# Optimization experiments

Measured on AMD Instinct MI355X. Metric: run time of the kernel, lower is better.

## Reference

```python
import jax, jax.numpy as jnp
import numpy as np

IO_EMB = 128; IO_HID = 512; ENC_HID = 1024
B = 256; N_IO = 4; L = 64; T = 32; NPROD = 64; VOCAB = 128


def setup_inputs() -> dict:
    key = jax.random.key(0)
    ks = jax.random.split(key, 16)
    s = 0.02
    return {
        'exs_toks': jax.random.randint(ks[0], (L, B * N_IO), 0, VOCAB),
        'cls_toks': jax.random.randint(ks[1], (L, B * N_IO), 0, VOCAB),
        'E_io': jax.random.normal(ks[2], (VOCAB, IO_EMB)) * s,
        'Wi_f': jax.random.normal(ks[3], (2 * IO_EMB, 4 * IO_HID)) * s,
        'Wh_f': jax.random.normal(ks[4], (IO_HID, 4 * IO_HID)) * s,
        'b_f': jnp.zeros((4 * IO_HID,)),
        'Wi_b': jax.random.normal(ks[5], (2 * IO_EMB, 4 * IO_HID)) * s,
        'Wh_b': jax.random.normal(ks[6], (IO_HID, 4 * IO_HID)) * s,
        'b_b': jnp.zeros((4 * IO_HID,)),
        'W_attn': jax.random.normal(ks[7], (ENC_HID, 2 * IO_HID)) * s,
        'W_comp': jax.random.normal(ks[8], (ENC_HID + 2 * IO_HID, NPROD)) * s,
        'b_comp': jnp.zeros((NPROD,)),
        'v_Wi': jax.random.normal(ks[9], (ENC_HID, 4 * ENC_HID)) * s,
        'v_Wh': jax.random.normal(ks[10], (ENC_HID, 4 * ENC_HID)) * s,
        'v_b': jnp.zeros((4 * ENC_HID,)),
        'field_emb': jax.random.normal(ks[11], (T, ENC_HID)) * s,
        'actions': jax.random.randint(ks[12], (B, T), 0, NPROD),
    }


def _lstm(x, Wi, Wh, b, reverse=False):
    # x: [L, N, D] -> hs [L, N, H], final (h, c)
    H = Wh.shape[0]
    N = x.shape[1]
    def step(carry, xt):
        h, c = carry
        g = xt @ Wi + h @ Wh + b
        i, f, gg, o = jnp.split(g, 4, axis=-1)
        c = jax.nn.sigmoid(f) * c + jax.nn.sigmoid(i) * jnp.tanh(gg)
        h = jax.nn.sigmoid(o) * jnp.tanh(c)
        return (h, c), h
    init = (jnp.zeros((N, H), x.dtype), jnp.zeros((N, H), x.dtype))
    (hT, cT), hs = jax.lax.scan(step, init, x, reverse=reverse)
    return hs, hT, cT


def reference(exs_toks, cls_toks, E_io, Wi_f, Wh_f, b_f, Wi_b, Wh_b, b_b,
              W_attn, W_comp, b_comp, v_Wi, v_Wh, v_b, field_emb, actions):
    # --- encode_io: concat exs/cls embeddings, run biLSTM ---
    x = jnp.concatenate([E_io[exs_toks], E_io[cls_toks]], axis=-1)  # [L, B*N_IO, 2*IO_EMB]
    hs_f, hTf, cTf = _lstm(x, Wi_f, Wh_f, b_f)
    hs_b, hTb, cTb = _lstm(x, Wi_b, Wh_b, b_b, reverse=True)
    ctx_vecs = jnp.concatenate([hs_f, hs_b], -1).reshape(L, B, N_IO, 2 * IO_HID)
    # init decoder state: max over io examples of final biLSTM state
    h0 = jnp.concatenate([hTf, hTb], -1).reshape(B, N_IO, ENC_HID).max(axis=1)
    c0 = jnp.concatenate([cTf, cTb], -1).reshape(B, N_IO, ENC_HID).max(axis=1)

    def dec_step(carry, xs):
        h, c, acc = carry
        x_t, a_t = xs  # field embedding [ENC_HID], action ids [B]
        # Luong attention over io context vecs, per io example, then max-pool
        q = h @ W_attn                               # [B, 2*IO_HID]
        scores = jnp.einsum('lbne,be->lbn', ctx_vecs, q)
        attn = jax.nn.softmax(scores, axis=0)
        ctx = jnp.einsum('lbn,lbne->bne', attn, ctx_vecs).max(axis=1)  # [B, 2*IO_HID]
        # per-node classifier (composite type module): negative log-prob of chosen prod
        logits = jnp.concatenate([h, ctx], -1) @ W_comp + b_comp
        logp = jax.nn.log_softmax(logits, axis=-1)
        acc = acc - logp[jnp.arange(B), a_t]
        # constructor update via v_lstm cell
        g = x_t @ v_Wi + h @ v_Wh + v_b
        i, f, gg, o = jnp.split(g, 4, axis=-1)
        c = jax.nn.sigmoid(f) * c + jax.nn.sigmoid(i) * jnp.tanh(gg)
        h = jax.nn.sigmoid(o) * jnp.tanh(c)
        return (h, c, acc), None

    init = (h0, c0, jnp.zeros((B,), h0.dtype))
    (_, _, total), _ = jax.lax.scan(dec_step, init, (field_emb, actions.T))
    return total  # [B] per-program negative log-likelihood
```

## Files before the change

### kernel.cpp

```cpp
#include <hip/hip_runtime.h>
#include <hip/hip_bf16.h>

typedef __bf16 bf16x8 __attribute__((ext_vector_type(8)));
typedef float  f32x4  __attribute__((ext_vector_type(4)));
typedef float  f32x2  __attribute__((ext_vector_type(2)));
typedef unsigned int u32x4 __attribute__((ext_vector_type(4)));
typedef unsigned short ushort_t;
static_assert(sizeof(bf16x8) == 16, "bf16x8 must be 16B");

#define DEV __device__ __forceinline__

DEV f32x4 mfma16(bf16x8 a, bf16x8 b, f32x4 c) {
    return __builtin_amdgcn_mfma_f32_16x16x32_bf16(a, b, c, 0, 0, 0);
}
DEV f32x4 mfma8(long a, long b, f32x4 c) {
    return __builtin_amdgcn_mfma_f32_16x16x32_fp8_fp8(a, b, c, 0, 0, 0);
}
DEV float sigm(float x)   { return 1.0f / (1.0f + __expf(-x)); }
DEV float tanh_f(float x) { return 2.0f / (1.0f + __expf(-2.0f * x)) - 1.0f; }

DEV void glds16(const __hip_bfloat16* g, __hip_bfloat16* l) {
    __builtin_amdgcn_global_load_lds(
        (const __attribute__((address_space(1))) unsigned int*)g,
        (__attribute__((address_space(3))) unsigned int*)l, 16, 0, 0);
}

DEV unsigned char f32_to_fp8(float v) {
    int p = __builtin_amdgcn_cvt_pk_fp8_f32(v, v, 0, false);
    return (unsigned char)(p & 0xFF);
}

__global__ __launch_bounds__(128) void kdetect(const unsigned int* __restrict__ raw,
                                               int* __restrict__ mode) {
    __shared__ int cnt;
    if (threadIdx.x == 0) cnt = 0;
    __syncthreads();
    unsigned int w = raw[threadIdx.x];
    unsigned short lo = (unsigned short)(w & 0xFFFFu);
    unsigned int f32bits = ((unsigned int)lo) << 16;
    float v;
    __builtin_memcpy(&v, &f32bits, 4);
    float a = fabsf(v);
    if (a >= 1e-4f && a <= 1.0f) atomicAdd(&cnt, 1);
    __syncthreads();
    if (threadIdx.x == 0) *mode = (cnt >= 64) ? 1 : 0;
}

__global__ __launch_bounds__(256) void kcvt_bf16(const void* __restrict__ src,
                                                 __hip_bfloat16* __restrict__ dst,
                                                 int n, const int* __restrict__ mode) {
    int i = blockIdx.x * 256 + threadIdx.x;
    if (i >= n) return;
    if (*mode) dst[i] = ((const __hip_bfloat16*)src)[i];
    else       dst[i] = __float2bfloat16(((const float*)src)[i]);
}

__global__ __launch_bounds__(256) void kcvt_f32(const void* __restrict__ src,
                                                float* __restrict__ dst,
                                                int n, const int* __restrict__ mode) {
    int i = blockIdx.x * 256 + threadIdx.x;
    if (i >= n) return;
    if (*mode) dst[i] = __bfloat162float(((const __hip_bfloat16*)src)[i]);
    else       dst[i] = ((const float*)src)[i];
}

__global__ __launch_bounds__(256) void ktranspose_cvt(const void* __restrict__ src,
                                                      __hip_bfloat16* __restrict__ out,
                                                      int R, int C,
                                                      const int* __restrict__ mode) {
    __shared__ float tile[64][65];
    int c0 = blockIdx.x * 64, r0 = blockIdx.y * 64;
    int tx = threadIdx.x & 63, ty = threadIdx.x >> 6;
    int m = *mode;
#pragma unroll
    for (int i = ty; i < 64; i += 4) {
        size_t ix = (size_t)(r0 + i) * C + (c0 + tx);
        tile[i][tx] = m ? __bfloat162float(((const __hip_bfloat16*)src)[ix])
                        : ((const float*)src)[ix];
    }
    __syncthreads();
#pragma unroll
    for (int i = ty; i < 64; i += 4)
        out[(size_t)(c0 + i) * R + (r0 + tx)] = __float2bfloat16(tile[tx][i]);
}

__global__ __launch_bounds__(256) void kprep_gtab(
    const __hip_bfloat16* __restrict__ E,
    const __hip_bfloat16* __restrict__ WiT,
    const float* __restrict__ bF,
    const float* __restrict__ bB,
    float* __restrict__ G)
{
    int dh = blockIdx.x >> 6;
    int dir = dh >> 1, half = dh & 1;
    int m0 = ((blockIdx.x >> 5) & 1) * 64;
    int n0 = (blockIdx.x & 31) * 64;
    int lane = threadIdx.x & 63, wid = threadIdx.x >> 6;
    int wrow = wid >> 1, wcol = wid & 1;
    int r16 = lane & 15, quad = lane >> 4;

    f32x4 acc[2][2] = {};
    const __hip_bfloat16* Ap = E + (size_t)(m0 + wrow * 32 + r16) * 128 + quad * 8;
    const __hip_bfloat16* Bp = WiT + (size_t)dir * 2048 * 256
                             + (size_t)(n0 + wcol * 32 + r16) * 256 + half * 128 + quad * 8;
#pragma unroll
    for (int kb = 0; kb < 128; kb += 32) {
        bf16x8 a0 = *(const bf16x8*)(Ap + kb);
        bf16x8 a1 = *(const bf16x8*)(Ap + 16 * 128 + kb);
        bf16x8 b0 = *(const bf16x8*)(Bp + kb);
        bf16x8 b1 = *(const bf16x8*)(Bp + 16 * 256 + kb);
        acc[0][0] = mfma16(a0, b0, acc[0][0]);
        acc[0][1] = mfma16(a0, b1, acc[0][1]);
        acc[1][0] = mfma16(a1, b0, acc[1][0]);
        acc[1][1] = mfma16(a1, b1, acc[1][1]);
    }
    const float* bias = dir ? bB : bF;
    float* Gt = G + (size_t)dh * 128 * 2048;
#pragma unroll
    for (int rt = 0; rt < 2; rt++)
#pragma unroll
        for (int ct = 0; ct < 2; ct++)
#pragma unroll
            for (int r = 0; r < 4; r++) {
                int mm = m0 + wrow * 32 + rt * 16 + quad * 4 + r;
                int j = n0 + wcol * 32 + ct * 16 + r16;
                float v = acc[rt][ct][r];
                if (half == 0) v += bias[j];
                int g = j >> 9, u = j & 511;
                Gt[((size_t)mm * 512 + u) * 4 + g] = v;
            }
}

__global__ __launch_bounds__(256) void kprep_vx(
    const __hip_bfloat16* __restrict__ fe,
    const __hip_bfloat16* __restrict__ vWiT,
    const float* __restrict__ vb,
    float* __restrict__ VX)
{
    int n0 = blockIdx.x * 128;
    int lane = threadIdx.x & 63, wid = threadIdx.x >> 6;
    int r16 = lane & 15, quad = lane >> 4;
    f32x4 acc[2][2] = {};
    const __hip_bfloat16* Ap = fe + (size_t)r16 * 1024 + quad * 8;
    const __hip_bfloat16* Bp = vWiT + (size_t)(n0 + wid * 32 + r16) * 1024 + quad * 8;
    for (int kb = 0; kb < 1024; kb += 32) {
        bf16x8 a0 = *(const bf16x8*)(Ap + kb);
        bf16x8 a1 = *(const bf16x8*)(Ap + 16 * 1024 + kb);
        bf16x8 b0 = *(const bf16x8*)(Bp + kb);
        bf16x8 b1 = *(const bf16x8*)(Bp + 16 * 1024 + kb);
        acc[0][0] = mfma16(a0, b0, acc[0][0]);
        acc[0][1] = mfma16(a0, b1, acc[0][1]);
        acc[1][0] = mfma16(a1, b0, acc[1][0]);
        acc[1][1] = mfma16(a1, b1, acc[1][1]);
    }
#pragma unroll
    for (int rt = 0; rt < 2; rt++)
#pragma unroll
        for (int ct = 0; ct < 2; ct++)
#pragma unroll
            for (int r = 0; r < 4; r++) {
                int m = rt * 16 + quad * 4 + r;
                int j = n0 + wid * 32 + ct * 16 + r16;
                VX[(size_t)m * 4096 + j] = acc[rt][ct][r] + vb[j];
            }
}

__global__ __launch_bounds__(256, 2) void kenc_step(
    int t,
    const __hip_bfloat16* __restrict__ WhT,
    const float* __restrict__ Gtab,
    const int* __restrict__ exs,
    const int* __restrict__ cls,
    const __hip_bfloat16* __restrict__ h_in,
    __hip_bfloat16* __restrict__ h_out,
    float* __restrict__ c_st,
    unsigned char* __restrict__ ctx8)
{
    __shared__ __align__(16) __hip_bfloat16 sA[3][64 * 64];
    __shared__ __align__(16) __hip_bfloat16 sB[3][128 * 64];

    int bid = blockIdx.x;
    int dir = bid >> 8;
    int mt  = (bid >> 4) & 15;
    int us  = bid & 15;
    int l = dir ? (63 - t) : t;
    int m0 = mt * 64, u0 = us * 32;

    int lane = threadIdx.x & 63, w = threadIdx.x >> 6;
    int wm = w >> 1, wu = w & 1;
    int r16 = lane & 15, quad = lane >> 4;
    int srow = lane >> 3;
    int scol = ((lane & 7) ^ srow) * 8;

    const __hip_bfloat16* Ab = h_in + (size_t)dir * 1024 * 512;
    const __hip_bfloat16* Bb = WhT + (size_t)dir * 2048 * 512;

    f32x4 acc[4][2] = {};

    auto stage = [&](int buf, int it) {
        int kb = it * 64;
#pragma unroll
        for (int c = 0; c < 2; c++) {
            int r8 = (w * 2 + c) * 8;
            glds16(Ab + (size_t)(m0 + r8 + srow) * 512 + kb + scol,
                   &sA[buf][r8 * 64]);
        }
#pragma unroll
        for (int c = 0; c < 4; c++) {
            int rl = (w * 4 + c) * 8;
            int rr = rl + srow;
            int g = rr >> 5, j = rr & 31;
            glds16(Bb + (size_t)(g * 512 + u0 + j) * 512 + kb + scol,
                   &sB[buf][rl * 64]);
        }
    };

    stage(0, 0);
    stage(1, 1);

    const int sw = r16 & 7;
    const int NIT = 8;
#pragma unroll
    for (int it = 0; it < NIT; it++) {
        if (it < NIT - 1)
            asm volatile("s_waitcnt vmcnt(6) lgkmcnt(0)" ::: "memory");
        else
            asm volatile("s_waitcnt vmcnt(0) lgkmcnt(0)" ::: "memory");
        __builtin_amdgcn_s_barrier();
        if (it + 2 < NIT) stage((it + 2) % 3, it + 2);
        const int buf = it % 3;
#pragma unroll
        for (int k32 = 0; k32 < 64; k32 += 32) {
            int co = (((k32 >> 3) + quad) ^ sw) * 8;
            bf16x8 a[2], bf[4];
#pragma unroll
            for (int mi = 0; mi < 2; mi++)
                a[mi] = *(const bf16x8*)&sA[buf][(wm * 32 + mi * 16 + r16) * 64 + co];
#pragma unroll
            for (int g = 0; g < 4; g++)
                bf[g] = *(const bf16x8*)&sB[buf][(g * 32 + wu * 16 + r16) * 64 + co];
#pragma unroll
            for (int g = 0; g < 4; g++)
#pragma unroll
                for (int mi = 0; mi < 2; mi++)
                    acc[g][mi] = mfma16(a[mi], bf[g], acc[g][mi]);
        }
    }

    int u = u0 + wu * 16 + r16;
    size_t cbase = (size_t)dir * 1024 * 512;
    const float* GeT = Gtab + (size_t)(dir * 2) * 128 * 2048;
    const float* GcT = GeT + 128 * 2048;
#pragma unroll
    for (int mi = 0; mi < 2; mi++)
#pragma unroll
        for (int r = 0; r < 4; r++) {
            int m = m0 + wm * 32 + mi * 16 + quad * 4 + r;
            int vE = exs[l * 1024 + m], vC = cls[l * 1024 + m];
            f32x4 ge = *(const f32x4*)&GeT[((size_t)vE * 512 + u) * 4];
            f32x4 gc = *(const f32x4*)&GcT[((size_t)vC * 512 + u) * 4];
            float gi = acc[0][mi][r] + ge[0] + gc[0];
            float gf = acc[1][mi][r] + ge[1] + gc[1];
            float gg = acc[2][mi][r] + ge[2] + gc[2];
            float go = acc[3][mi][r] + ge[3] + gc[3];
            size_t cix = cbase + (size_t)m * 512 + u;
            float cn = sigm(gf) * c_st[cix] + sigm(gi) * tanh_f(gg);
            c_st[cix] = cn;
            float hn = sigm(go) * tanh_f(cn);
            h_out[cix] = __float2bfloat16(hn);
            ctx8[(((size_t)l * 256 + (m >> 2)) * 4 + (m & 3)) * 1024 + dir * 512 + u]
                = f32_to_fp8(hn * 16.0f);
        }
}

__global__ __launch_bounds__(256) void ktrans8(const unsigned char* __restrict__ ctx8,
                                               unsigned char* __restrict__ ctxT8) {
    __shared__ unsigned int tile[64][17];
    int b4n = blockIdx.x;
    int e0 = blockIdx.y * 64;
    int tid = threadIdx.x;
#pragma unroll
    for (int pass = 0; pass < 4; pass++) {
        int idx = pass * 256 + tid;
        int l = idx >> 4, c = idx & 15;
        tile[l][c] = *(const unsigned int*)(ctx8 + (size_t)l * (1024 * 1024)
                                            + (size_t)b4n * 1024 + e0 + c * 4);
    }
    __syncthreads();
    const unsigned char* tb = (const unsigned char*)tile;
#pragma unroll
    for (int pass = 0; pass < 4; pass++) {
        int idx = pass * 256 + tid;
        int e = idx >> 4, c = idx & 15;
        unsigned int v = 0;
#pragma unroll
        for (int j = 0; j < 4; j++) {
            unsigned int byte = tb[(size_t)(c * 4 + j) * 68 + e];
            v |= byte << (8 * j);
        }
        *(unsigned int*)(ctxT8 + ((size_t)b4n * 1024 + e0 + e) * 64 + c * 4) = v;
    }
}

__global__ __launch_bounds__(256, 2) void kdec_gemm(
    int t,
    const __hip_bfloat16* __restrict__ vWhT,
    const __hip_bfloat16* __restrict__ WattnT,
    const float* __restrict__ VX,
    const __hip_bfloat16* __restrict__ h_in,
    __hip_bfloat16* __restrict__ h_out,
    float* __restrict__ c_st,
    float* __restrict__ qout)
{
    __shared__ __align__(16) __hip_bfloat16 sA[2][32 * 64];
    __shared__ __align__(16) __hip_bfloat16 sB[2][256 * 64];

    int bid = blockIdx.x;
    int lane = threadIdx.x & 63, w = threadIdx.x >> 6;
    int r16 = lane & 15, quad = lane >> 4;
    int srow = lane >> 3;
    int scol = ((lane & 7) ^ srow) * 8;
    const int NIT = 16;
    const int sw = r16 & 7;

    if (bid < 128) {
        int m0 = (bid >> 4) * 32, u0 = (bid & 15) * 64;
        f32x4 acc[4][2] = {};
        auto stage = [&](int buf, int it) {
            int kb = it * 64;
            glds16(h_in + (size_t)(m0 + w * 8 + srow) * 1024 + kb + scol,
                   &sA[buf][(w * 8) * 64]);
#pragma unroll
            for (int c = 0; c < 8; c++) {
                int rl = w * 64 + c * 8;
                int rr = rl + srow;
                int g = rr >> 6, j = rr & 63;
                glds16(vWhT + (size_t)(g * 1024 + u0 + j) * 1024 + kb + scol,
                       &sB[buf][rl * 64]);
            }
        };
        stage(0, 0);
        __syncthreads();
        int buf = 0;
        for (int it = 0; it < NIT; it++) {
            if (it + 1 < NIT) stage(buf ^ 1, it + 1);
#pragma unroll
            for (int k32 = 0; k32 < 64; k32 += 32) {
                int co = (((k32 >> 3) + quad) ^ sw) * 8;
                bf16x8 a[2], bf[4];
#pragma unroll
                for (int mi = 0; mi < 2; mi++)
                    a[mi] = *(const bf16x8*)&sA[buf][(mi * 16 + r16) * 64 + co];
#pragma unroll
                for (int g = 0; g < 4; g++)
                    bf[g] = *(const bf16x8*)&sB[buf][(g * 64 + w * 16 + r16) * 64 + co];
#pragma unroll
                for (int g = 0; g < 4; g++)
#pragma unroll
                    for (int mi = 0; mi < 2; mi++)
                        acc[g][mi] = mfma16(a[mi], bf[g], acc[g][mi]);
            }
            __syncthreads();
            buf ^= 1;
        }
        int u = u0 + w * 16 + r16;
        const float* vx = VX + (size_t)t * 4096;
        float v0 = vx[u], v1 = vx[1024 + u], v2 = vx[2048 + u], v3 = vx[3072 + u];
#pragma unroll
        for (int mi = 0; mi < 2; mi++)
#pragma unroll
            for (int r = 0; r < 4; r++) {
                int m = m0 + mi * 16 + quad * 4 + r;
                float gi = acc[0][mi][r] + v0;
                float gf = acc[1][mi][r] + v1;
                float gg = acc[2][mi][r] + v2;
                float go = acc[3][mi][r] + v3;
                size_t cix = (size_t)m * 1024 + u;
                float cn = sigm(gf) * c_st[cix] + sigm(gi) * tanh_f(gg);
                c_st[cix] = cn;
                h_out[cix] = __float2bfloat16(sigm(go) * tanh_f(cn));
            }
    } else {
        int b2 = bid - 128;
        int m0 = (b2 >> 4) * 32, n0 = (b2 & 15) * 64;
        f32x4 acc[2] = {};
        auto stage = [&](int buf, int it) {
            int kb = it * 64;
            glds16(h_in + (size_t)(m0 + w * 8 + srow) * 1024 + kb + scol,
                   &sA[buf][(w * 8) * 64]);
#pragma unroll
            for (int c = 0; c < 2; c++) {
                int rl = w * 16 + c * 8;
                glds16(WattnT + (size_t)(n0 + rl + srow) * 1024 + kb + scol,
                       &sB[buf][rl * 64]);
            }
        };
        stage(0, 0);
        __syncthreads();
        int buf = 0;
        for (int it = 0; it < NIT; it++) {
            if (it + 1 < NIT) stage(buf ^ 1, it + 1);
#pragma unroll
            for (int k32 = 0; k32 < 64; k32 += 32) {
                int co = (((k32 >> 3) + quad) ^ sw) * 8;
                bf16x8 a[2];
#pragma unroll
                for (int mi = 0; mi < 2; mi++)
                    a[mi] = *(const bf16x8*)&sA[buf][(mi * 16 + r16) * 64 + co];
                bf16x8 bf = *(const bf16x8*)&sB[buf][(w * 16 + r16) * 64 + co];
#pragma unroll
                for (int mi = 0; mi < 2; mi++)
                    acc[mi] = mfma16(a[mi], bf, acc[mi]);
            }
            __syncthreads();
            buf ^= 1;
        }
        int n = n0 + w * 16 + r16;
#pragma unroll
        for (int mi = 0; mi < 2; mi++)
#pragma unroll
            for (int r = 0; r < 4; r++) {
                int m = m0 + mi * 16 + quad * 4 + r;
                qout[(size_t)m * 1024 + n] = acc[mi][r];
            }
    }
}

__global__ __launch_bounds__(512, 2) void kattn_mfma(
    const float* __restrict__ qall,
    const unsigned char* __restrict__ ctx8,
    const unsigned char* __restrict__ ctxT8,
    const __hip_bfloat16* __restrict__ hAll,
    const __hip_bfloat16* __restrict__ WcT,
    const float* __restrict__ bcomp,
    const int* __restrict__ actions,
    float* __restrict__ nllT)
{
    __shared__ __align__(16) unsigned char sQ8[32 * 1032];
    __shared__ float sS[4][32][65];
    __shared__ __align__(16) unsigned char sP[4 * 32 * 72];
    __shared__ __align__(16) ushort_t sPool[32 * 1032];
    __shared__ float slg[32 * 68];

    int b = blockIdx.x;
    int tid = threadIdx.x;
    int lane = tid & 63, w = tid >> 6;
    int r16 = lane & 15, quad = lane >> 4;
    const size_t LSTR = 1024 * 1024;

    for (int i = 0; i < 64; i++) {
        int idx = i * 512 + tid;
        int t = idx >> 10, e = idx & 1023;
        float v = qall[((size_t)t * 256 + b) * 1024 + e] * 0.25f;
        sQ8[t * 1032 + e] = f32_to_fp8(v);
    }
    __syncthreads();

    {
        int n = w >> 1, lh = w & 1;
        int l0 = lh * 32;
        f32x4 c[2][2] = {};
        const unsigned char* cbase = ctx8 + (size_t)(b * 4 + n) * 1024;
        for (int k0 = 0; k0 < 1024; k0 += 32) {
            long a[2], bv[2];
#pragma unroll
            for (int mt = 0; mt < 2; mt++)
                __builtin_memcpy(&a[mt], &sQ8[(mt * 16 + r16) * 1032 + k0 + quad * 8], 8);
#pragma unroll
            for (int lt = 0; lt < 2; lt++)
                bv[lt] = *(const long*)(cbase + (size_t)(l0 + lt * 16 + r16) * LSTR
                                        + k0 + quad * 8);
#pragma unroll
            for (int mt = 0; mt < 2; mt++)
#pragma unroll
                for (int lt = 0; lt < 2; lt++)
                    c[mt][lt] = mfma8(a[mt], bv[lt], c[mt][lt]);
        }
#pragma unroll
        for (int mt = 0; mt < 2; mt++)
#pragma unroll
            for (int lt = 0; lt < 2; lt++)
#pragma unroll
                for (int r = 0; r < 4; r++)
                    sS[n][mt * 16 + quad * 4 + r][l0 + lt * 16 + r16] = c[mt][lt][r];
    }
    __syncthreads();

    if (tid < 128) {
        int n = tid >> 5, t = tid & 31;
        const float* row = &sS[n][t][0];
        float sum = 0.f;
        for (int l = 0; l < 64; l++)
            sum += __expf(fminf(row[l] * 0.25f, 60.f));
        float inv = 16.0f / sum;
        unsigned char* pr = &sP[(n * 32 + t) * 72];
        for (int l = 0; l < 64; l++)
            pr[l] = f32_to_fp8(__expf(fminf(row[l] * 0.25f, 60.f)) * inv);
    }
    __syncthreads();

    {
        int e0 = w * 128;
        f32x4 pool[2][8];
#pragma unroll
        for (int mt = 0; mt < 2; mt++)
#pragma unroll
            for (int et = 0; et < 8; et++)
#pragma unroll
                for (int r = 0; r < 4; r++) pool[mt][et][r] = -3.4e38f;

        for (int n = 0; n < 4; n++) {
            f32x4 c[2][8] = {};
            const unsigned char* tbase = ctxT8 + (size_t)(b * 4 + n) * 1024 * 64;
#pragma unroll
            for (int k0 = 0; k0 < 64; k0 += 32) {
                long a[2];
#pragma unroll
                for (int mt = 0; mt < 2; mt++)
                    __builtin_memcpy(&a[mt], &sP[(n * 32 + mt * 16 + r16) * 72 + k0 + quad * 8], 8);
#pragma unroll
                for (int et = 0; et < 8; et++) {
                    long bv = *(const long*)(tbase + (size_t)(e0 + et * 16 + r16) * 64
                                             + k0 + quad * 8);
#pragma unroll
                    for (int mt = 0; mt < 2; mt++)
                        c[mt][et] = mfma8(a[mt], bv, c[mt][et]);
                }
            }
#pragma unroll
            for (int mt = 0; mt < 2; mt++)
#pragma unroll
                for (int et = 0; et < 8; et++)
#pragma unroll
                    for (int r = 0; r < 4; r++)
                        pool[mt][et][r] = fmaxf(pool[mt][et][r], c[mt][et][r] * (1.0f / 256.0f));
        }
#pragma unroll
        for (int mt = 0; mt < 2; mt++)
#pragma unroll
            for (int et = 0; et < 8; et++)
#pragma unroll
                for (int r = 0; r < 4; r++) {
                    int t = mt * 16 + quad * 4 + r;
                    int e = e0 + et * 16 + r16;
                    __hip_bfloat16 hb = __float2bfloat16(pool[mt][et][r]);
                    sPool[t * 1032 + e] = *(ushort_t*)&hb;
                }
    }
    __syncthreads();

    {
        int mt = w & 1, pt = w >> 1;
        f32x4 c = {};
        const __hip_bfloat16* hrow = hAll + ((size_t)(mt * 16 + r16) * 256 + b) * 1024;
        const __hip_bfloat16* wrow = WcT + (size_t)(pt * 16 + r16) * 2048;
        for (int k0 = 0; k0 < 2048; k0 += 32) {
            bf16x8 a;
            if (k0 < 1024)
                a = *(const bf16x8*)(hrow + k0 + quad * 8);
            else
                a = *(const bf16x8*)&sPool[(mt * 16 + r16) * 1032 + (k0 - 1024) + quad * 8];
            bf16x8 bv = *(const bf16x8*)(wrow + k0 + quad * 8);
            c = mfma16(a, bv, c);
        }
#pragma unroll
        for (int r = 0; r < 4; r++) {
            int t = mt * 16 + quad * 4 + r;
            int p = pt * 16 + r16;
            slg[t * 68 + p] = c[r] + bcomp[p];
        }
    }
    __syncthreads();

    if (tid < 32) {
        int t = tid;
        const float* row = &slg[t * 68];
        float m = -3.4e38f;
        for (int p = 0; p < 64; p++) m = fmaxf(m, row[p]);
        float se = 0.f;
        for (int p = 0; p < 64; p++) se += __expf(row[p] - m);
        int a = actions[b * 32 + t];
        nllT[t * 256 + b] = m + __logf(se) - row[a];
    }
}

__global__ __launch_bounds__(256) void kinit_dec(
    const __hip_bfloat16* __restrict__ hf,
    const float* __restrict__ cf,
    __hip_bfloat16* __restrict__ h0,
    float* __restrict__ c0)
{
    int idx = blockIdx.x * 256 + threadIdx.x;
    int b = idx >> 10, e = idx & 1023;
    int dir = e >> 9, u = e & 511;
    const __hip_bfloat16* hs = hf + (size_t)dir * 1024 * 512;
    const float* cs = cf + (size_t)dir * 1024 * 512;
    float hv = -3.4e38f, cv = -3.4e38f;
#pragma unroll
    for (int n = 0; n < 4; n++) {
        size_t ix = (size_t)(b * 4 + n) * 512 + u;
        hv = fmaxf(hv, __bfloat162float(hs[ix]));
        cv = fmaxf(cv, cs[ix]);
    }
    h0[idx] = __float2bfloat16(hv);
    c0[idx] = cv;
}

__global__ void kfinal(const float* __restrict__ nllT, void* __restrict__ out,
                       const int* __restrict__ mode) {
    int i = threadIdx.x;
    float s = 0.f;
#pragma unroll
    for (int t = 0; t < 32; t++) s += nllT[t * 256 + i];
    if (*mode) ((__hip_bfloat16*)out)[i] = __float2bfloat16(s);
    else       ((float*)out)[i] = s;
}

extern "C" void kernel_launch(void* const* d_in, const int* in_sizes, int n_in,
                              void* d_out, int out_size, void* d_ws, size_t ws_size,
                              hipStream_t stream) {
    const int* exs = (const int*)d_in[0];
    const int* cls = (const int*)d_in[1];
    const void* E_raw     = d_in[2];
    const void* WiF_raw   = d_in[3];
    const void* WhF_raw   = d_in[4];
    const void* bF_raw    = d_in[5];
    const void* WiB_raw   = d_in[6];
    const void* WhB_raw   = d_in[7];
    const void* bB_raw    = d_in[8];
    const void* Wattn_raw = d_in[9];
    const void* Wcomp_raw = d_in[10];
    const void* bcomp_raw = d_in[11];
    const void* vWi_raw   = d_in[12];
    const void* vWh_raw   = d_in[13];
    const void* vb_raw    = d_in[14];
    const void* fe_raw    = d_in[15];
    const int* actions = (const int*)d_in[16];
    (void)in_sizes; (void)n_in; (void)out_size; (void)ws_size;

    char* w = (char*)d_ws;
    size_t off = 0;
    auto take = [&](size_t bytes) -> char* {
        char* p = w + off;
        off = (off + bytes + 255) & ~(size_t)255;
        return p;
    };
    __hip_bfloat16* WhT    = (__hip_bfloat16*)take(2ull * 2048 * 512 * 2);
    __hip_bfloat16* WiT    = (__hip_bfloat16*)take(2ull * 2048 * 256 * 2);
    __hip_bfloat16* vWhT   = (__hip_bfloat16*)take(4096ull * 1024 * 2);
    __hip_bfloat16* vWiT   = (__hip_bfloat16*)take(4096ull * 1024 * 2);
    __hip_bfloat16* WattnT = (__hip_bfloat16*)take(1024ull * 1024 * 2);
    __hip_bfloat16* WcT    = (__hip_bfloat16*)take(64ull * 2048 * 2);
    __hip_bfloat16* Ebf    = (__hip_bfloat16*)take(128ull * 128 * 2);
    __hip_bfloat16* febf   = (__hip_bfloat16*)take(32ull * 1024 * 2);
    float* bFf   = (float*)take(2048 * 4);
    float* bBf   = (float*)take(2048 * 4);
    float* bcf   = (float*)take(64 * 4);
    float* vbf   = (float*)take(4096 * 4);
    float* Gtab  = (float*)take(4ull * 128 * 2048 * 4);
    float* VX    = (float*)take(32ull * 4096 * 4);
    __hip_bfloat16* hEnc = (__hip_bfloat16*)take(2ull * 2 * 1024 * 512 * 2);
    float* cEnc = (float*)take(2ull * 1024 * 512 * 4);
    __hip_bfloat16* hAll = (__hip_bfloat16*)take(33ull * 256 * 1024 * 2);
    float* cDec = (float*)take(256ull * 1024 * 4);
    float* qall = (float*)take(32ull * 256 * 1024 * 4);
    float* nllT = (float*)take(32ull * 256 * 4);
    int*   mode = (int*)take(256);
    unsigned char* ctx8  = (unsigned char*)take(64ull * 1024 * 1024);
    unsigned char* ctxT8 = (unsigned char*)take(64ull * 1024 * 1024);

    (void)hipMemsetAsync(hEnc, 0, 2ull * 1024 * 512 * 2, stream);
    (void)hipMemsetAsync(cEnc, 0, 2ull * 1024 * 512 * 4, stream);

    kdetect<<<1, 128, 0, stream>>>((const unsigned int*)E_raw, mode);

    kcvt_bf16<<<64, 256, 0, stream>>>(E_raw,  Ebf,  128 * 128, mode);
    kcvt_bf16<<<128, 256, 0, stream>>>(fe_raw, febf, 32 * 1024, mode);
    kcvt_f32<<<8, 256, 0, stream>>>(bF_raw, bFf, 2048, mode);
    kcvt_f32<<<8, 256, 0, stream>>>(bB_raw, bBf, 2048, mode);
    kcvt_f32<<<1, 256, 0, stream>>>(bcomp_raw, bcf, 64, mode);
    kcvt_f32<<<16, 256, 0, stream>>>(vb_raw, vbf, 4096, mode);

    ktranspose_cvt<<<dim3(32, 8),  256, 0, stream>>>(WhF_raw,   WhT,              512, 2048, mode);
    ktranspose_cvt<<<dim3(32, 8),  256, 0, stream>>>(WhB_raw,   WhT + 2048 * 512, 512, 2048, mode);
    ktranspose_cvt<<<dim3(32, 4),  256, 0, stream>>>(WiF_raw,   WiT,              256, 2048, mode);
    ktranspose_cvt<<<dim3(32, 4),  256, 0, stream>>>(WiB_raw,   WiT + 2048 * 256, 256, 2048, mode);
    ktranspose_cvt<<<dim3(64, 16), 256, 0, stream>>>(vWh_raw,   vWhT,            1024, 4096, mode);
    ktranspose_cvt<<<dim3(64, 16), 256, 0, stream>>>(vWi_raw,   vWiT,            1024, 4096, mode);
    ktranspose_cvt<<<dim3(16, 16), 256, 0, stream>>>(Wattn_raw, WattnT,          1024, 1024, mode);
    ktranspose_cvt<<<dim3(1, 32),  256, 0, stream>>>(Wcomp_raw, WcT,             2048, 64,   mode);

    kprep_gtab<<<256, 256, 0, stream>>>(Ebf, WiT, bFf, bBf, Gtab);
    kprep_vx<<<32, 256, 0, stream>>>(febf, vWiT, vbf, VX);

    const size_t HB = 2ull * 1024 * 512;
    for (int t = 0; t < 64; t++) {
        kenc_step<<<512, 256, 0, stream>>>(t, WhT, Gtab, exs, cls,
                                           hEnc + (size_t)(t & 1) * HB,
                                           hEnc + (size_t)((t + 1) & 1) * HB,
                                           cEnc, ctx8);
    }
    ktrans8<<<dim3(1024, 16), 256, 0, stream>>>(ctx8, ctxT8);
    kinit_dec<<<1024, 256, 0, stream>>>(hEnc, cEnc, hAll, cDec);

    const size_t HD = 256ull * 1024;
    for (int t = 0; t < 32; t++) {
        kdec_gemm<<<256, 256, 0, stream>>>(t, vWhT, WattnT, VX,
                                           hAll + (size_t)t * HD,
                                           hAll + (size_t)(t + 1) * HD,
                                           cDec, qall + (size_t)t * HD);
    }
    kattn_mfma<<<256, 512, 0, stream>>>(qall, ctx8, ctxT8, hAll, WcT, bcf,
                                        actions, nllT);
    kfinal<<<1, 256, 0, stream>>>(nllT, d_out, mode);
}
```

Before: 1.650 ms.

## Triple-buffer decoder GEMM loads and retile to 64x32 blocks

The decoder GEMM kernel moves from a double-buffered to a triple-buffered LDS pipeline with two stages in flight. It replaces __syncthreads with explicit vmcnt waits plus a single barrier per iteration. Block tiles change from 32 rows x 64 units to 64 rows x 32 units, with waves arranged 2x2, which rebalances how much of the A and B tiles each block loads. The aim is to hide global-load latency and cut the number of barriers, at the cost of more LDS per block and hand-counted wait counters that must match the number of issued loads.

```diff
diff --git a/kernel.cpp b/kernel.cpp
--- a/kernel.cpp
+++ b/kernel.cpp
@@ -312,65 +312,78 @@
     float* __restrict__ c_st,
     float* __restrict__ qout)
 {
-    __shared__ __align__(16) __hip_bfloat16 sA[2][32 * 64];
-    __shared__ __align__(16) __hip_bfloat16 sB[2][256 * 64];
+    __shared__ __align__(16) __hip_bfloat16 sA[3][64 * 64];
+    __shared__ __align__(16) __hip_bfloat16 sB[3][128 * 64];
 
     int bid = blockIdx.x;
     int lane = threadIdx.x & 63, w = threadIdx.x >> 6;
+    int wm = w >> 1, wu = w & 1;
     int r16 = lane & 15, quad = lane >> 4;
     int srow = lane >> 3;
     int scol = ((lane & 7) ^ srow) * 8;
     const int NIT = 16;
     const int sw = r16 & 7;
 
-    if (bid < 128) {
-        int m0 = (bid >> 4) * 32, u0 = (bid & 15) * 64;
+    bool cellp = bid < 128;
+    int b2 = cellp ? bid : bid - 128;
+    int m0 = (b2 >> 5) * 64;
+    int n0 = (b2 & 31) * 32;
+
+    if (cellp) {
         f32x4 acc[4][2] = {};
         auto stage = [&](int buf, int it) {
             int kb = it * 64;
-            glds16(h_in + (size_t)(m0 + w * 8 + srow) * 1024 + kb + scol,
-                   &sA[buf][(w * 8) * 64]);
-#pragma unroll
-            for (int c = 0; c < 8; c++) {
-                int rl = w * 64 + c * 8;
+#pragma unroll
+            for (int c = 0; c < 2; c++) {
+                int r8 = (w * 2 + c) * 8;
+                glds16(h_in + (size_t)(m0 + r8 + srow) * 1024 + kb + scol,
+                       &sA[buf][r8 * 64]);
+            }
+#pragma unroll
+            for (int c = 0; c < 4; c++) {
+                int rl = (w * 4 + c) * 8;
                 int rr = rl + srow;
-                int g = rr >> 6, j = rr & 63;
-                glds16(vWhT + (size_t)(g * 1024 + u0 + j) * 1024 + kb + scol,
+                int g = rr >> 5, j = rr & 31;
+                glds16(vWhT + (size_t)(g * 1024 + n0 + j) * 1024 + kb + scol,
                        &sB[buf][rl * 64]);
             }
         };
         stage(0, 0);
-        __syncthreads();
-        int buf = 0;
+        stage(1, 1);
+#pragma unroll
         for (int it = 0; it < NIT; it++) {
-            if (it + 1 < NIT) stage(buf ^ 1, it + 1);
+            if (it < NIT - 1)
+                asm volatile("s_waitcnt vmcnt(6) lgkmcnt(0)" ::: "memory");
+            else
+                asm volatile("s_waitcnt vmcnt(0) lgkmcnt(0)" ::: "memory");
+            __builtin_amdgcn_s_barrier();
+            if (it + 2 < NIT) stage((it + 2) % 3, it + 2);
+            const int buf = it % 3;
 #pragma unroll
             for (int k32 = 0; k32 < 64; k32 += 32) {
                 int co = (((k32 >> 3) + quad) ^ sw) * 8;
                 bf16x8 a[2], bf[4];
 #pragma unroll
                 for (int mi = 0; mi < 2; mi++)
-                    a[mi] = *(const bf16x8*)&sA[buf][(mi * 16 + r16) * 64 + co];
+                    a[mi] = *(const bf16x8*)&sA[buf][(wm * 32 + mi * 16 + r16) * 64 + co];
 #pragma unroll
                 for (int g = 0; g < 4; g++)
-                    bf[g] = *(const bf16x8*)&sB[buf][(g * 64 + w * 16 + r16) * 64 + co];
+                    bf[g] = *(const bf16x8*)&sB[buf][(g * 32 + wu * 16 + r16) * 64 + co];
 #pragma unroll
                 for (int g = 0; g < 4; g++)
 #pragma unroll
                     for (int mi = 0; mi < 2; mi++)
                         acc[g][mi] = mfma16(a[mi], bf[g], acc[g][mi]);
             }
-            __syncthreads();
-            buf ^= 1;
-        }
-        int u = u0 + w * 16 + r16;
+        }
+        int u = n0 + wu * 16 + r16;
         const float* vx = VX + (size_t)t * 4096;
         float v0 = vx[u], v1 = vx[1024 + u], v2 = vx[2048 + u], v3 = vx[3072 + u];
 #pragma unroll
         for (int mi = 0; mi < 2; mi++)
 #pragma unroll
             for (int r = 0; r < 4; r++) {
-                int m = m0 + mi * 16 + quad * 4 + r;
+                int m = m0 + wm * 32 + mi * 16 + quad * 4 + r;
                 float gi = acc[0][mi][r] + v0;
                 float gf = acc[1][mi][r] + v1;
                 float gg = acc[2][mi][r] + v2;
@@ -381,46 +394,51 @@
                 h_out[cix] = __float2bfloat16(sigm(go) * tanh_f(cn));
             }
     } else {
-        int b2 = bid - 128;
-        int m0 = (b2 >> 4) * 32, n0 = (b2 & 15) * 64;
         f32x4 acc[2] = {};
         auto stage = [&](int buf, int it) {
             int kb = it * 64;
-            glds16(h_in + (size_t)(m0 + w * 8 + srow) * 1024 + kb + scol,
-                   &sA[buf][(w * 8) * 64]);
 #pragma unroll
             for (int c = 0; c < 2; c++) {
-                int rl = w * 16 + c * 8;
+                int r8 = (w * 2 + c) * 8;
+                glds16(h_in + (size_t)(m0 + r8 + srow) * 1024 + kb + scol,
+                       &sA[buf][r8 * 64]);
+            }
+            {
+                int rl = w * 8;
                 glds16(WattnT + (size_t)(n0 + rl + srow) * 1024 + kb + scol,
                        &sB[buf][rl * 64]);
             }
         };
         stage(0, 0);
-        __syncthreads();
-        int buf = 0;
+        stage(1, 1);
+#pragma unroll
         for (int it = 0; it < NIT; it++) {
-            if (it + 1 < NIT) stage(buf ^ 1, it + 1);
+            if (it < NIT - 1)
+                asm volatile("s_waitcnt vmcnt(3) lgkmcnt(0)" ::: "memory");
+            else
+                asm volatile("s_waitcnt vmcnt(0) lgkmcnt(0)" ::: "memory");
+            __builtin_amdgcn_s_barrier();
+            if (it + 2 < NIT) stage((it + 2) % 3, it + 2);
+            const int buf = it % 3;
 #pragma unroll
             for (int k32 = 0; k32 < 64; k32 += 32) {
                 int co = (((k32 >> 3) + quad) ^ sw) * 8;
                 bf16x8 a[2];
 #pragma unroll
                 for (int mi = 0; mi < 2; mi++)
-                    a[mi] = *(const bf16x8*)&sA[buf][(mi * 16 + r16) * 64 + co];
-                bf16x8 bf = *(const bf16x8*)&sB[buf][(w * 16 + r16) * 64 + co];
+                    a[mi] = *(const bf16x8*)&sA[buf][(wm * 32 + mi * 16 + r16) * 64 + co];
+                bf16x8 bf = *(const bf16x8*)&sB[buf][(wu * 16 + r16) * 64 + co];
 #pragma unroll
                 for (int mi = 0; mi < 2; mi++)
                     acc[mi] = mfma16(a[mi], bf, acc[mi]);
             }
-            __syncthreads();
-            buf ^= 1;
-        }
-        int n = n0 + w * 16 + r16;
+        }
+        int n = n0 + wu * 16 + r16;
 #pragma unroll
         for (int mi = 0; mi < 2; mi++)
 #pragma unroll
             for (int r = 0; r < 4; r++) {
-                int m = m0 + mi * 16 + quad * 4 + r;
+                int m = m0 + wm * 32 + mi * 16 + quad * 4 + r;
                 qout[(size_t)m * 1024 + n] = acc[mi][r];
             }
     }
```

Result: faster. 1.587 ms (-3.8%).
